# Optimization experiments

Hardware: AMD Instinct MI355X
Metric: run time of the kernel (lower is better)

## Reference

```python
import jax, jax.numpy as jnp
import numpy as np

B, N, C, H = 8, 1024, 768, 12
D = C // H  # head_dim = 64
SCALE = D ** -0.5
EPS = 1e-5  # nn.LayerNorm default


def layer_norm(x, gamma, beta):
    # normalize over last dim (head_dim)
    mu = jnp.mean(x, axis=-1, keepdims=True)
    var = jnp.var(x, axis=-1, keepdims=True)
    return (x - mu) * jax.lax.rsqrt(var + EPS) * gamma + beta


def setup_inputs() -> dict:
    key = jax.random.key(0)
    ks = jax.random.split(key, 5)
    s = 0.02
    return {
        "x": jax.random.normal(ks[0], (B, N, C), jnp.float32),
        "qkv_w": jax.random.normal(ks[1], (3 * C, C), jnp.float32) * s,
        "qkv_b": jax.random.normal(ks[2], (3 * C,), jnp.float32) * s,
        "q_gamma": jnp.ones((D,), jnp.float32),
        "q_beta": jnp.zeros((D,), jnp.float32),
        "k_gamma": jnp.ones((D,), jnp.float32),
        "k_beta": jnp.zeros((D,), jnp.float32),
        "proj_w": jax.random.normal(ks[3], (C, C), jnp.float32) * s,
        "proj_b": jax.random.normal(ks[4], (C,), jnp.float32) * s,
    }


def reference(x, qkv_w, qkv_b, q_gamma, q_beta, k_gamma, k_beta, proj_w, proj_b):
    Bx, Nx, Cx = x.shape
    qkv = x @ qkv_w.T + qkv_b                       # [B,N,3C]
    qkv = qkv.reshape(Bx, Nx, 3, H, D).transpose(2, 0, 3, 1, 4)  # [3,B,H,N,D]
    q, k, v = qkv[0], qkv[1], qkv[2]
    q = layer_norm(q, q_gamma, q_beta) * SCALE
    k = layer_norm(k, k_gamma, k_beta)
    attn = jax.nn.softmax(jnp.einsum('bhnd,bhmd->bhnm', q, k), axis=-1)  # [B,H,N,N]
    # attn_drop is identity (p=0, eval)
    out = jnp.einsum('bhnm,bhmd->bhnd', attn, v)    # [B,H,N,D]
    out = out.transpose(0, 2, 1, 3).reshape(Bx, Nx, Cx)
    out = out @ proj_w.T + proj_b                   # proj_drop identity
    return out, attn
```

## Files before the change

kernel.cpp:

```cpp
#include <hip/hip_runtime.h>
#include <hip/hip_bf16.h>
#include <stdint.h>

typedef __bf16 bf16_t;
typedef __bf16 bf16x8 __attribute__((ext_vector_type(8)));
typedef float f32x4 __attribute__((ext_vector_type(4)));

#define DEV static __device__ __forceinline__

DEV f32x4 mfma16(bf16x8 a, bf16x8 b, f32x4 c) {
  return __builtin_amdgcn_mfma_f32_16x16x32_bf16(a, b, c, 0, 0, 0);
}

DEV void gll16(const void* g, void* l) {
  __builtin_amdgcn_global_load_lds(
      (const __attribute__((address_space(1))) uint32_t*)g,
      (__attribute__((address_space(3))) uint32_t*)l, 16, 0, 0);
}

DEV int swz128(int row, int c16) {
  return (row << 7) + (((c16 ^ row) & 7) << 4);
}
DEV int swzel128(int row, int col) {
  return (row << 7) + ((((col >> 3) ^ row) & 7) << 4) + ((col & 7) << 1);
}

DEV void stage_tile_gll(const bf16_t* g, char* lds, int wave, int lane) {
  int r0 = wave * 8 + (lane >> 3);
  int b = lane & 7;
#pragma unroll
  for (int q = 0; q < 2; q++) {
    int row = q * 32 + r0;
    gll16(g + ((long)row << 6) + (((b ^ row) & 7) << 3),
          lds + q * 4096 + wave * 1024);
  }
}

__global__ void __launch_bounds__(256)
cast_all(const float* __restrict__ x, bf16_t* __restrict__ ox,
         const float* __restrict__ w1, bf16_t* __restrict__ ow1,
         const float* __restrict__ w2, bf16_t* __restrict__ ow2) {
  long i = (long)(blockIdx.x * 256 + threadIdx.x) * 8;
  const float* s; bf16_t* d; long off;
  if (i < 6291456L)      { s = x;  d = ox;  off = i; }
  else if (i < 8060928L) { s = w1; d = ow1; off = i - 6291456L; }
  else if (i < 8650752L) { s = w2; d = ow2; off = i - 8060928L; }
  else return;
  float4 a = *(const float4*)(s + off);
  float4 b = *(const float4*)(s + off + 4);
  bf16x8 v;
  v[0] = (bf16_t)a.x; v[1] = (bf16_t)a.y; v[2] = (bf16_t)a.z; v[3] = (bf16_t)a.w;
  v[4] = (bf16_t)b.x; v[5] = (bf16_t)b.y; v[6] = (bf16_t)b.z; v[7] = (bf16_t)b.w;
  *(bf16x8*)(d + off) = v;
}

template<int OUT_BF16>
__global__ void __launch_bounds__(256, 2)
gemm_bt(const bf16_t* __restrict__ A, const bf16_t* __restrict__ Bw,
        const float* __restrict__ bias, void* __restrict__ Cout,
        int M, int N, int K) {
  __shared__ __align__(16) char As[8192];
  __shared__ __align__(16) char Bs[8192];
  const int tid = threadIdx.x;
  const int lane = tid & 63;
  const int wave = tid >> 6;
  const int wr = wave >> 1, wc = wave & 1;
  const int tileM = blockIdx.y << 7;
  const int tileN = blockIdx.x << 7;
  const int lrow = lane & 15, lk = lane >> 4;

  f32x4 acc[4][4];
  f32x4 z = {0.f, 0.f, 0.f, 0.f};
#pragma unroll
  for (int m = 0; m < 4; m++)
#pragma unroll
    for (int n = 0; n < 4; n++) acc[m][n] = z;

  const int srow = wave * 16 + (lane >> 2);
  const int sb = lane & 3;
  const bf16_t* Asrc0 = A + (long)(tileM + srow) * K + sb * 8;
  const bf16_t* Asrc1 = A + (long)(tileM + 64 + srow) * K + sb * 8;
  const bf16_t* Bsrc0 = Bw + (long)(tileN + srow) * K + sb * 8;
  const bf16_t* Bsrc1 = Bw + (long)(tileN + 64 + srow) * K + sb * 8;
  char* Adst = As + wave * 1024;
  char* Bdst = Bs + wave * 1024;

  for (int k0 = 0; k0 < K; k0 += 32) {
    __syncthreads();
    gll16(Asrc0 + k0, Adst);
    gll16(Asrc1 + k0, Adst + 4096);
    gll16(Bsrc0 + k0, Bdst);
    gll16(Bsrc1 + k0, Bdst + 4096);
    __syncthreads();
    bf16x8 af[4], bfr[4];
#pragma unroll
    for (int m = 0; m < 4; m++)
      af[m] = *(const bf16x8*)(As + (wr * 64 + m * 16 + lrow) * 64 + lk * 16);
#pragma unroll
    for (int n = 0; n < 4; n++)
      bfr[n] = *(const bf16x8*)(Bs + (wc * 64 + n * 16 + lrow) * 64 + lk * 16);
#pragma unroll
    for (int m = 0; m < 4; m++)
#pragma unroll
      for (int n = 0; n < 4; n++)
        acc[m][n] = mfma16(af[m], bfr[n], acc[m][n]);
  }

  const int rg = lk;
#pragma unroll
  for (int n = 0; n < 4; n++) {
    int col = tileN + wc * 64 + n * 16 + lrow;
    float bv = bias[col];
#pragma unroll
    for (int m = 0; m < 4; m++) {
      long row0 = tileM + wr * 64 + m * 16 + rg * 4;
#pragma unroll
      for (int r = 0; r < 4; r++) {
        float v = acc[m][n][r] + bv;
        if (OUT_BF16) ((bf16_t*)Cout)[(row0 + r) * N + col] = (bf16_t)v;
        else          ((float*)Cout)[(row0 + r) * N + col] = v;
      }
    }
  }
}

__global__ void __launch_bounds__(256)
ln_qkv(const bf16_t* __restrict__ qkv,
       const float* __restrict__ qg, const float* __restrict__ qb,
       const float* __restrict__ kg, const float* __restrict__ kb,
       bf16_t* __restrict__ qT) {
  const int tid = threadIdx.x;
  long row = (long)blockIdx.x * 32 + (tid >> 3);
  int d0 = (tid & 7) * 8;
  int h = (int)(row % 12);
  long bn3 = row / 12;
  int t = (int)(bn3 % 3);
  long bn = bn3 / 3;

  bf16x8 xv = *(const bf16x8*)(qkv + row * 64 + d0);
  float x[8];
  float s = 0.f, s2 = 0.f;
#pragma unroll
  for (int j = 0; j < 8; j++) { x[j] = (float)xv[j]; s += x[j]; s2 += x[j] * x[j]; }
  s += __shfl_xor(s, 1);  s2 += __shfl_xor(s2, 1);
  s += __shfl_xor(s, 2);  s2 += __shfl_xor(s2, 2);
  s += __shfl_xor(s, 4);  s2 += __shfl_xor(s2, 4);
  float mu = s * (1.f / 64.f);
  float var = s2 * (1.f / 64.f) - mu * mu;
  float rstd = rsqrtf(var + 1e-5f);

  bf16x8 yv;
  if (t == 0) {
#pragma unroll
    for (int j = 0; j < 8; j++)
      yv[j] = (bf16_t)(((x[j] - mu) * rstd * qg[d0 + j] + qb[d0 + j]) * 0.125f);
  } else if (t == 1) {
#pragma unroll
    for (int j = 0; j < 8; j++)
      yv[j] = (bf16_t)((x[j] - mu) * rstd * kg[d0 + j] + kb[d0 + j]);
  } else {
    yv = xv;
  }
  long b = bn >> 10, n = bn & 1023;
  long dst = (long)t * 6291456 + (((b * 12 + h) << 10) + n) * 64 + d0;
  *(bf16x8*)(qT + dst) = yv;
}

__global__ void __launch_bounds__(256, 2)
attn_kernel(const bf16_t* __restrict__ qT, float* __restrict__ attn_out,
            bf16_t* __restrict__ out_heads) {
  const int tid = threadIdx.x;
  const int lane = tid & 63;
  const int wave = tid >> 6;
  const int qt = blockIdx.x;
  const int bh = blockIdx.y;
  const int b = bh / 12, h = bh - b * 12;

  const bf16_t* Qg = qT + (long)bh * 65536;
  const bf16_t* Kg = qT + 6291456L + (long)bh * 65536;
  const bf16_t* Vg = qT + 12582912L + (long)bh * 65536;

  __shared__ __align__(16) char Ks[16384];
  __shared__ __align__(16) char Vt[8192];
  __shared__ __align__(16) char QP[8192];
  __shared__ __align__(16) float ATs[64 * 68];

  const int lrow = lane & 15;
  const int lk = lane >> 4;

  stage_tile_gll(Qg + ((long)qt << 12), QP, wave, lane);
  stage_tile_gll(Kg, Ks, wave, lane);
  __syncthreads();

  bf16x8 qf[2];
  qf[0] = *(const bf16x8*)(QP + swz128(wave * 16 + lrow, lk));
  qf[1] = *(const bf16x8*)(QP + swz128(wave * 16 + lrow, 4 + lk));

  auto computeS = [&](const char* Kb, f32x4 sfr[4]) {
    f32x4 z = {0.f, 0.f, 0.f, 0.f};
    sfr[0] = z; sfr[1] = z; sfr[2] = z; sfr[3] = z;
#pragma unroll
    for (int kk = 0; kk < 2; kk++)
#pragma unroll
      for (int f = 0; f < 4; f++) {
        bf16x8 kf = *(const bf16x8*)(Kb + swz128(f * 16 + lrow, kk * 4 + lk));
        sfr[f] = mfma16(qf[kk], kf, sfr[f]);
      }
  };

  float m_r[4], l_r[4];
#pragma unroll
  for (int r = 0; r < 4; r++) { m_r[r] = -1e30f; l_r[r] = 0.f; }

  for (int kt = 0; kt < 16; kt++) {
    if (kt < 15)
      stage_tile_gll(Kg + ((long)(kt + 1) << 12), Ks + ((kt + 1) & 1) * 8192, wave, lane);
    f32x4 sfr[4];
    computeS(Ks + (kt & 1) * 8192, sfr);
#pragma unroll
    for (int r = 0; r < 4; r++) {
      float mx = fmaxf(fmaxf(sfr[0][r], sfr[1][r]), fmaxf(sfr[2][r], sfr[3][r]));
      float nm = fmaxf(m_r[r], mx);
      float acc = __expf(sfr[0][r] - nm) + __expf(sfr[1][r] - nm) +
                  __expf(sfr[2][r] - nm) + __expf(sfr[3][r] - nm);
      l_r[r] = l_r[r] * __expf(m_r[r] - nm) + acc;
      m_r[r] = nm;
    }
    __syncthreads();
  }

  float il[4];
#pragma unroll
  for (int r = 0; r < 4; r++) {
#pragma unroll
    for (int ofs = 1; ofs <= 8; ofs <<= 1) {
      float om = __shfl_xor(m_r[r], ofs);
      float ol = __shfl_xor(l_r[r], ofs);
      float nm = fmaxf(m_r[r], om);
      l_r[r] = l_r[r] * __expf(m_r[r] - nm) + ol * __expf(om - nm);
      m_r[r] = nm;
    }
    il[r] = 1.0f / l_r[r];
  }

  f32x4 of[4];
  {
    f32x4 z = {0.f, 0.f, 0.f, 0.f};
    of[0] = z; of[1] = z; of[2] = z; of[3] = z;
  }
  char* Pw = QP + wave * 2048;
  float* attn_base = attn_out + (long)bh * 1048576;

  stage_tile_gll(Kg, Ks, wave, lane);
  const int vk = lane;
  const int vdg = wave;
  bf16x8 vr0 = *(const bf16x8*)(Vg + ((long)vk << 6) + vdg * 16);
  bf16x8 vr1 = *(const bf16x8*)(Vg + ((long)vk << 6) + vdg * 16 + 8);

  for (int kt = 0; kt < 16; kt++) {
    __syncthreads();
#pragma unroll
    for (int j = 0; j < 8; j++) {
      *(bf16_t*)(Vt + swzel128(vdg * 16 + j, vk)) = vr0[j];
      *(bf16_t*)(Vt + swzel128(vdg * 16 + 8 + j, vk)) = vr1[j];
    }
    f32x4 sfr[4];
    computeS(Ks + (kt & 1) * 8192, sfr);
#pragma unroll
    for (int f = 0; f < 4; f++)
#pragma unroll
      for (int r = 0; r < 4; r++) {
        float p = __expf(sfr[f][r] - m_r[r]) * il[r];
        int lr = lk * 4 + r;
        int col = f * 16 + lrow;
        ATs[(wave * 16 + lr) * 68 + col] = p;
        *(bf16_t*)(Pw + swzel128(lr, col)) = (bf16_t)p;
      }
    __syncthreads();
    if (kt < 15) {
      stage_tile_gll(Kg + ((long)(kt + 1) << 12), Ks + ((kt + 1) & 1) * 8192, wave, lane);
      const bf16_t* vp = Vg + ((long)((kt + 1) * 64 + vk) << 6) + vdg * 16;
      vr0 = *(const bf16x8*)(vp);
      vr1 = *(const bf16x8*)(vp + 8);
    }
#pragma unroll
    for (int kk = 0; kk < 2; kk++) {
      bf16x8 pf = *(const bf16x8*)(Pw + swz128(lrow, kk * 4 + lk));
#pragma unroll
      for (int f = 0; f < 4; f++) {
        bf16x8 vf = *(const bf16x8*)(Vt + swz128(f * 16 + lrow, kk * 4 + lk));
        of[f] = mfma16(pf, vf, of[f]);
      }
    }
    float* ab = attn_base + ((long)(qt * 64) << 10) + kt * 64;
#pragma unroll
    for (int i = 0; i < 4; i++) {
      int idx = i * 256 + tid;
      int row = idx >> 4, c4 = idx & 15;
      f32x4 v = *(const f32x4*)(ATs + row * 68 + c4 * 4);
      __builtin_nontemporal_store(v, (f32x4*)(ab + ((long)row << 10) + c4 * 4));
    }
  }

#pragma unroll
  for (int f = 0; f < 4; f++)
#pragma unroll
    for (int r = 0; r < 4; r++) {
      int nrow = qt * 64 + wave * 16 + lk * 4 + r;
      int d = f * 16 + lrow;
      out_heads[((long)b * 1024 + nrow) * 768 + h * 64 + d] = (bf16_t)of[f][r];
    }
}

extern "C" void kernel_launch(void* const* d_in, const int* in_sizes, int n_in,
                              void* d_out, int out_size, void* d_ws, size_t ws_size,
                              hipStream_t stream) {
  (void)in_sizes; (void)n_in; (void)out_size; (void)ws_size;
  const float* x       = (const float*)d_in[0];
  const float* qkv_w   = (const float*)d_in[1];
  const float* qkv_b   = (const float*)d_in[2];
  const float* q_gamma = (const float*)d_in[3];
  const float* q_beta  = (const float*)d_in[4];
  const float* k_gamma = (const float*)d_in[5];
  const float* k_beta  = (const float*)d_in[6];
  const float* proj_w  = (const float*)d_in[7];
  const float* proj_b  = (const float*)d_in[8];
  float* out = (float*)d_out;

  char* ws = (char*)d_ws;
  bf16_t* x_bf   = (bf16_t*)(ws);
  bf16_t* wqkv   = (bf16_t*)(ws + 12582912L);
  bf16_t* wproj  = (bf16_t*)(ws + 16121856L);
  bf16_t* qkvbuf = (bf16_t*)(ws + 17301504L);
  bf16_t* qT     = (bf16_t*)(ws + 55050240L);
  bf16_t* out_heads = qkvbuf;

  cast_all<<<4224, 256, 0, stream>>>(x, x_bf, qkv_w, wqkv, proj_w, wproj);
  gemm_bt<1><<<dim3(18, 64), 256, 0, stream>>>(x_bf, wqkv, qkv_b, qkvbuf, 8192, 2304, 768);
  ln_qkv<<<9216, 256, 0, stream>>>(qkvbuf, q_gamma, q_beta, k_gamma, k_beta, qT);
  attn_kernel<<<dim3(16, 96), 256, 0, stream>>>(qT, out + 6291456L, out_heads);
  gemm_bt<0><<<dim3(6, 64), 256, 0, stream>>>(out_heads, wproj, proj_b, out, 8192, 768, 768);
}
```

Before: 219.6 us.

## Fuse QK LayerNorm and head-major scatter into QKV GEMM epilogue; use exp2 softmax

```diff
diff --git a/kernel.cpp b/kernel.cpp
--- a/kernel.cpp
+++ b/kernel.cpp
@@ -54,10 +54,115 @@
   *(bf16x8*)(d + off) = v;
 }
 
-template<int OUT_BF16>
+#define C1Q 0.1803368801111244f
+
+__global__ void __launch_bounds__(256, 2)
+gemm_qkv_ln(const bf16_t* __restrict__ A, const bf16_t* __restrict__ Bw,
+            const float* __restrict__ bias,
+            const float* __restrict__ qg, const float* __restrict__ qb,
+            const float* __restrict__ kg, const float* __restrict__ kb,
+            bf16_t* __restrict__ qT, int M, int N, int K) {
+  __shared__ __align__(16) char As[8192];
+  __shared__ __align__(16) char Bs[8192];
+  const int tid = threadIdx.x;
+  const int lane = tid & 63;
+  const int wave = tid >> 6;
+  const int wr = wave >> 1, wc = wave & 1;
+  const int tileM = blockIdx.y << 7;
+  const int tileN = blockIdx.x << 7;
+  const int lrow = lane & 15, lk = lane >> 4;
+
+  f32x4 acc[4][4];
+  f32x4 z = {0.f, 0.f, 0.f, 0.f};
+#pragma unroll
+  for (int m = 0; m < 4; m++)
+#pragma unroll
+    for (int n = 0; n < 4; n++) acc[m][n] = z;
+
+  const int srow = wave * 16 + (lane >> 2);
+  const int sb = lane & 3;
+  const bf16_t* Asrc0 = A + (long)(tileM + srow) * K + sb * 8;
+  const bf16_t* Asrc1 = A + (long)(tileM + 64 + srow) * K + sb * 8;
+  const bf16_t* Bsrc0 = Bw + (long)(tileN + srow) * K + sb * 8;
+  const bf16_t* Bsrc1 = Bw + (long)(tileN + 64 + srow) * K + sb * 8;
+  char* Adst = As + wave * 1024;
+  char* Bdst = Bs + wave * 1024;
+
+  for (int k0 = 0; k0 < K; k0 += 32) {
+    __syncthreads();
+    gll16(Asrc0 + k0, Adst);
+    gll16(Asrc1 + k0, Adst + 4096);
+    gll16(Bsrc0 + k0, Bdst);
+    gll16(Bsrc1 + k0, Bdst + 4096);
+    __syncthreads();
+    bf16x8 af[4], bfr[4];
+#pragma unroll
+    for (int m = 0; m < 4; m++)
+      af[m] = *(const bf16x8*)(As + (wr * 64 + m * 16 + lrow) * 64 + lk * 16);
+#pragma unroll
+    for (int n = 0; n < 4; n++)
+      bfr[n] = *(const bf16x8*)(Bs + (wc * 64 + n * 16 + lrow) * 64 + lk * 16);
+#pragma unroll
+    for (int m = 0; m < 4; m++)
+#pragma unroll
+      for (int n = 0; n < 4; n++)
+        acc[m][n] = mfma16(af[m], bfr[n], acc[m][n]);
+  }
+
+  const int t = tileN / 768;
+  const int hh = ((tileN % 768) >> 6) + wc;
+  float g[4], be[4], bv[4];
+#pragma unroll
+  for (int n = 0; n < 4; n++) bv[n] = bias[tileN + wc * 64 + n * 16 + lrow];
+  if (t == 0) {
+#pragma unroll
+    for (int n = 0; n < 4; n++) {
+      int d = n * 16 + lrow;
+      g[n] = qg[d] * C1Q; be[n] = qb[d] * C1Q;
+    }
+  } else if (t == 1) {
+#pragma unroll
+    for (int n = 0; n < 4; n++) {
+      int d = n * 16 + lrow;
+      g[n] = kg[d]; be[n] = kb[d];
+    }
+  }
+
+#pragma unroll
+  for (int m = 0; m < 4; m++) {
+#pragma unroll
+    for (int r = 0; r < 4; r++) {
+      float v[4];
+#pragma unroll
+      for (int n = 0; n < 4; n++) v[n] = acc[m][n][r] + bv[n];
+      long row = tileM + wr * 64 + m * 16 + lk * 4 + r;
+      long bb = row >> 10, nseq = row & 1023;
+      bf16_t* dst = qT + (long)t * 6291456L + ((bb * 12 + hh) * 1024 + nseq) * 64;
+      if (t < 2) {
+        float s = v[0] + v[1] + v[2] + v[3];
+        float s2 = v[0]*v[0] + v[1]*v[1] + v[2]*v[2] + v[3]*v[3];
+#pragma unroll
+        for (int ofs = 1; ofs <= 8; ofs <<= 1) {
+          s  += __shfl_xor(s, ofs);
+          s2 += __shfl_xor(s2, ofs);
+        }
+        float mu = s * (1.f / 64.f);
+        float rstd = rsqrtf(s2 * (1.f / 64.f) - mu * mu + 1e-5f);
+#pragma unroll
+        for (int n = 0; n < 4; n++)
+          dst[n * 16 + lrow] = (bf16_t)((v[n] - mu) * rstd * g[n] + be[n]);
+      } else {
+#pragma unroll
+        for (int n = 0; n < 4; n++)
+          dst[n * 16 + lrow] = (bf16_t)v[n];
+      }
+    }
+  }
+}
+
 __global__ void __launch_bounds__(256, 2)
 gemm_bt(const bf16_t* __restrict__ A, const bf16_t* __restrict__ Bw,
-        const float* __restrict__ bias, void* __restrict__ Cout,
+        const float* __restrict__ bias, float* __restrict__ Cout,
         int M, int N, int K) {
   __shared__ __align__(16) char As[8192];
   __shared__ __align__(16) char Bs[8192];
@@ -115,55 +220,10 @@
     for (int m = 0; m < 4; m++) {
       long row0 = tileM + wr * 64 + m * 16 + rg * 4;
 #pragma unroll
-      for (int r = 0; r < 4; r++) {
-        float v = acc[m][n][r] + bv;
-        if (OUT_BF16) ((bf16_t*)Cout)[(row0 + r) * N + col] = (bf16_t)v;
-        else          ((float*)Cout)[(row0 + r) * N + col] = v;
-      }
-    }
-  }
-}
-
-__global__ void __launch_bounds__(256)
-ln_qkv(const bf16_t* __restrict__ qkv,
-       const float* __restrict__ qg, const float* __restrict__ qb,
-       const float* __restrict__ kg, const float* __restrict__ kb,
-       bf16_t* __restrict__ qT) {
-  const int tid = threadIdx.x;
-  long row = (long)blockIdx.x * 32 + (tid >> 3);
-  int d0 = (tid & 7) * 8;
-  int h = (int)(row % 12);
-  long bn3 = row / 12;
-  int t = (int)(bn3 % 3);
-  long bn = bn3 / 3;
-
-  bf16x8 xv = *(const bf16x8*)(qkv + row * 64 + d0);
-  float x[8];
-  float s = 0.f, s2 = 0.f;
-#pragma unroll
-  for (int j = 0; j < 8; j++) { x[j] = (float)xv[j]; s += x[j]; s2 += x[j] * x[j]; }
-  s += __shfl_xor(s, 1);  s2 += __shfl_xor(s2, 1);
-  s += __shfl_xor(s, 2);  s2 += __shfl_xor(s2, 2);
-  s += __shfl_xor(s, 4);  s2 += __shfl_xor(s2, 4);
-  float mu = s * (1.f / 64.f);
-  float var = s2 * (1.f / 64.f) - mu * mu;
-  float rstd = rsqrtf(var + 1e-5f);
-
-  bf16x8 yv;
-  if (t == 0) {
-#pragma unroll
-    for (int j = 0; j < 8; j++)
-      yv[j] = (bf16_t)(((x[j] - mu) * rstd * qg[d0 + j] + qb[d0 + j]) * 0.125f);
-  } else if (t == 1) {
-#pragma unroll
-    for (int j = 0; j < 8; j++)
-      yv[j] = (bf16_t)((x[j] - mu) * rstd * kg[d0 + j] + kb[d0 + j]);
-  } else {
-    yv = xv;
-  }
-  long b = bn >> 10, n = bn & 1023;
-  long dst = (long)t * 6291456 + (((b * 12 + h) << 10) + n) * 64 + d0;
-  *(bf16x8*)(qT + dst) = yv;
+      for (int r = 0; r < 4; r++)
+        Cout[(row0 + r) * N + col] = acc[m][n][r] + bv;
+    }
+  }
 }
 
 __global__ void __launch_bounds__(256, 2)
@@ -221,9 +281,9 @@
     for (int r = 0; r < 4; r++) {
       float mx = fmaxf(fmaxf(sfr[0][r], sfr[1][r]), fmaxf(sfr[2][r], sfr[3][r]));
       float nm = fmaxf(m_r[r], mx);
-      float acc = __expf(sfr[0][r] - nm) + __expf(sfr[1][r] - nm) +
-                  __expf(sfr[2][r] - nm) + __expf(sfr[3][r] - nm);
-      l_r[r] = l_r[r] * __expf(m_r[r] - nm) + acc;
+      float acc = exp2f(sfr[0][r] - nm) + exp2f(sfr[1][r] - nm) +
+                  exp2f(sfr[2][r] - nm) + exp2f(sfr[3][r] - nm);
+      l_r[r] = l_r[r] * exp2f(m_r[r] - nm) + acc;
       m_r[r] = nm;
     }
     __syncthreads();
@@ -237,7 +297,7 @@
       float om = __shfl_xor(m_r[r], ofs);
       float ol = __shfl_xor(l_r[r], ofs);
       float nm = fmaxf(m_r[r], om);
-      l_r[r] = l_r[r] * __expf(m_r[r] - nm) + ol * __expf(om - nm);
+      l_r[r] = l_r[r] * exp2f(m_r[r] - nm) + ol * exp2f(om - nm);
       m_r[r] = nm;
     }
     il[r] = 1.0f / l_r[r];
@@ -270,7 +330,7 @@
     for (int f = 0; f < 4; f++)
 #pragma unroll
       for (int r = 0; r < 4; r++) {
-        float p = __expf(sfr[f][r] - m_r[r]) * il[r];
+        float p = exp2f(sfr[f][r] - m_r[r]) * il[r];
         int lr = lk * 4 + r;
         int col = f * 16 + lrow;
         ATs[(wave * 16 + lr) * 68 + col] = p;
@@ -328,16 +388,16 @@
   float* out = (float*)d_out;
 
   char* ws = (char*)d_ws;
-  bf16_t* x_bf   = (bf16_t*)(ws);
-  bf16_t* wqkv   = (bf16_t*)(ws + 12582912L);
-  bf16_t* wproj  = (bf16_t*)(ws + 16121856L);
-  bf16_t* qkvbuf = (bf16_t*)(ws + 17301504L);
-  bf16_t* qT     = (bf16_t*)(ws + 55050240L);
-  bf16_t* out_heads = qkvbuf;
+  bf16_t* x_bf      = (bf16_t*)(ws);
+  bf16_t* wqkv      = (bf16_t*)(ws + 12582912L);
+  bf16_t* wproj     = (bf16_t*)(ws + 16121856L);
+  bf16_t* qT        = (bf16_t*)(ws + 17301504L);
+  bf16_t* out_heads = (bf16_t*)(ws + 55050240L);
 
   cast_all<<<4224, 256, 0, stream>>>(x, x_bf, qkv_w, wqkv, proj_w, wproj);
-  gemm_bt<1><<<dim3(18, 64), 256, 0, stream>>>(x_bf, wqkv, qkv_b, qkvbuf, 8192, 2304, 768);
-  ln_qkv<<<9216, 256, 0, stream>>>(qkvbuf, q_gamma, q_beta, k_gamma, k_beta, qT);
+  gemm_qkv_ln<<<dim3(18, 64), 256, 0, stream>>>(x_bf, wqkv, qkv_b,
+                                                q_gamma, q_beta, k_gamma, k_beta,
+                                                qT, 8192, 2304, 768);
   attn_kernel<<<dim3(16, 96), 256, 0, stream>>>(qT, out + 6291456L, out_heads);
-  gemm_bt<0><<<dim3(6, 64), 256, 0, stream>>>(out_heads, wproj, proj_b, out, 8192, 768, 768);
-}
+  gemm_bt<<<dim3(6, 64), 256, 0, stream>>>(out_heads, wproj, proj_b, out, 8192, 768, 768);
+}
```

Measured after the change: 219.8 us. About the same (+0.1%).
